# Optimization experiments

Hardware: AMD Instinct MI355X
Metric: run time of the kernel (lower is better)

The kernel has to match this reference:

```python
import jax, jax.numpy as jnp
import numpy as np

B, T, C = 2, 2048, 2048
H, HK = 16, 4          # n_head, n_kv_head (GQA)
HD = C // H            # head_dim = 128
EPS = 1e-6             # rms-norm eps


def _rope(x, cos, sin):
    # x: [B,T,h,d]; cos/sin: [T, d/2] (rotate-half RoPE)
    d2 = x.shape[-1] // 2
    x1, x2 = x[..., :d2], x[..., d2:]
    c = cos[None, :, None, :]
    s = sin[None, :, None, :]
    return jnp.concatenate([x1 * c - x2 * s, x1 * s + x2 * c], axis=-1)


def _rms(x):
    # weightless QK-norm (F.rms_norm over last dim)
    return x * jax.lax.rsqrt(jnp.mean(x * x, axis=-1, keepdims=True) + EPS)


def setup_inputs() -> dict:
    key = jax.random.key(0)
    ks = jax.random.split(key, 6)
    x = jax.random.normal(ks[0], (B, T, C), dtype=jnp.float32)
    # realistic RoPE tables
    inv_freq = 1.0 / (10000.0 ** (jnp.arange(0, HD, 2, dtype=jnp.float32) / HD))  # [HD/2]
    ang = jnp.arange(T, dtype=jnp.float32)[:, None] * inv_freq[None, :]           # [T, HD/2]
    cos, sin = jnp.cos(ang), jnp.sin(ang)
    std = 0.02
    Wq = jax.random.normal(ks[1], (C, H * HD), dtype=jnp.float32) * std
    Wk = jax.random.normal(ks[2], (C, HK * HD), dtype=jnp.float32) * std
    Wv = jax.random.normal(ks[3], (C, HK * HD), dtype=jnp.float32) * std
    Wproj = jax.random.normal(ks[4], (C, C), dtype=jnp.float32) * std
    mix1 = jnp.float32(1.0)
    mix2 = jnp.float32(0.5)
    return {"x": x, "cos": cos, "sin": sin, "Wq": Wq, "Wk": Wk, "Wv": Wv,
            "Wproj": Wproj, "mix1": mix1, "mix2": mix2}


def reference(x, cos, sin, Wq, Wk, Wv, Wproj, mix1, mix2):
    Bx, Tx, Cx = x.shape
    q = (x @ Wq).reshape(Bx, Tx, H, HD)
    k = (x @ Wk).reshape(Bx, Tx, HK, HD)
    v = (x @ Wv).reshape(Bx, Tx, HK, HD)
    q = _rms(_rope(q, cos, sin))
    k = _rms(_rope(k, cos, sin))
    q = q.transpose(0, 2, 1, 3)  # [B,H,T,D]
    k = k.transpose(0, 2, 1, 3)  # [B,HK,T,D]
    v = v.transpose(0, 2, 1, 3)
    rep = H // HK
    k = jnp.repeat(k, rep, axis=1)  # GQA repeat -> [B,H,T,D]
    v = jnp.repeat(v, rep, axis=1)
    att = jnp.einsum('bhqd,bhkd->bhqk', q, k) * (1.0 / np.sqrt(HD))
    mask = jnp.tril(jnp.ones((Tx, Tx), dtype=bool))
    att = jnp.where(mask[None, None], att, -jnp.inf)
    att = jax.nn.softmax(att, axis=-1)
    y1 = att @ v            # first-order attention output
    y2 = att @ y1           # second-order simplicial mixing (reuses att)
    y = mix1 * y1 + mix2 * y2
    y = y.transpose(0, 2, 1, 3).reshape(Bx, Tx, Cx)
    return y @ Wproj
```

## Files before the change

### kernel.cpp

```cpp
#include <hip/hip_runtime.h>
#include <hip/hip_bf16.h>
#include <cstdint>
#include <cstddef>

#define AS1 __attribute__((address_space(1)))
#define AS3 __attribute__((address_space(3)))

typedef __attribute__((ext_vector_type(8))) short bf16x8;
typedef __attribute__((ext_vector_type(4))) float f32x4;

__device__ __forceinline__ void gload_lds16(const void* g, void* l) {
  __builtin_amdgcn_global_load_lds((const AS1 void*)g, (AS3 void*)l, 16, 0, 0);
}

#define MFMA_BF16(A, B, C) __builtin_amdgcn_mfma_f32_16x16x32_bf16((A), (B), (C), 0, 0, 0)

#define QSCALE 0.12751744f
#define SMAX 16.5f

__device__ __forceinline__ uint32_t pk2(float a, float b) {
  uint32_t ua = (uint32_t)__builtin_bit_cast(unsigned short, __float2bfloat16(a));
  uint32_t ub = (uint32_t)__builtin_bit_cast(unsigned short, __float2bfloat16(b));
  return ua | (ub << 16);
}
// ... 150 lines not shown
#pragma unroll
    for (int qq = 0; qq < 16; ++qq)
      w[qq] = *(const uint2*)(CL4 + (((th * 16 + qq) * 133 + col) << 2));
    __hip_bfloat16* dstv = vb + (size_t)col * 2048 + t0 + th * 64;
#pragma unroll
    for (int e = 0; e < 8; ++e)
      *(uint4*)(dstv + e * 8) = make_uint4(w[2 * e].x, w[2 * e].y, w[2 * e + 1].x, w[2 * e + 1].y);
    return;
  }

  const int quad = tid >> 3, cp = tid & 7;
  const int tb = t0 + quad * 4;
  bf16x8 lov[4], hiv[4];
#pragma unroll
  for (int e = 0; e < 4; ++e) {
    lov[e] = *(const bf16x8*)(CL4 + ((quad * 133 + cp * 8 + e * 2) << 2));
    hiv[e] = *(const bf16x8*)(CL4 + ((quad * 133 + 64 + cp * 8 + e * 2) << 2));
  }
  const float oscale = (col0 < 2048) ? QSCALE : 1.0f;
  __hip_bfloat16* dstq = (col0 < 2048)
      ? qT + (size_t)(b * 16 + (col0 >> 7)) * 2048 * 128
      : kT + (size_t)(b * 4 + ((col0 - 2048) >> 7)) * 2048 * 128;

  float o1v[4][8], o2v[4][8], ssum[4];
#pragma unroll
  for (int rr = 0; rr < 4; ++rr) {
    const float* cb = cosb + (size_t)(tb + rr) * 64 + cp * 8;
    const float* sb = sinb + (size_t)(tb + rr) * 64 + cp * 8;
    float4 c0 = *(const float4*)cb, c1 = *(const float4*)(cb + 4);
    float4 s0 = *(const float4*)sb, s1 = *(const float4*)(sb + 4);
    float cc[8] = {c0.x, c0.y, c0.z, c0.w, c1.x, c1.y, c1.z, c1.w};
    float sn[8] = {s0.x, s0.y, s0.z, s0.w, s1.x, s1.y, s1.z, s1.w};
    float ss = 0.f;
#pragma unroll
    for (int e = 0; e < 4; ++e)
#pragma unroll
      for (int w2 = 0; w2 < 2; ++w2) {
        int pd = e * 2 + w2;
        float x1 = b2f((unsigned short)lov[e][w2 * 4 + rr]);
        float x2 = b2f((unsigned short)hiv[e][w2 * 4 + rr]);
        float a = x1 * cc[pd] - x2 * sn[pd];
        float bb = x1 * sn[pd] + x2 * cc[pd];
        o1v[rr][pd] = a;
        o2v[rr][pd] = bb;
        ss += a * a + bb * bb;
      }
    ssum[rr] = ss;
  }
#pragma unroll
  for (int rr = 0; rr < 4; ++rr) {
    float rn = rsqrtf(red8_sum(ssum[rr]) * (1.f / 128.f) + 1e-6f) * oscale;
    __hip_bfloat16* dr = dstq + (size_t)(tb + rr) * 128 + cp * 8;
    *(uint4*)dr = make_uint4(pk2(o1v[rr][0] * rn, o1v[rr][1] * rn),
                             pk2(o1v[rr][2] * rn, o1v[rr][3] * rn),
                             pk2(o1v[rr][4] * rn, o1v[rr][5] * rn),
                             pk2(o1v[rr][6] * rn, o1v[rr][7] * rn));
    *(uint4*)(dr + 64) = make_uint4(pk2(o2v[rr][0] * rn, o2v[rr][1] * rn),
                                    pk2(o2v[rr][2] * rn, o2v[rr][3] * rn),
                                    pk2(o2v[rr][4] * rn, o2v[rr][5] * rn),
                                    pk2(o2v[rr][6] * rn, o2v[rr][7] * rn));
  }
}

__global__ __launch_bounds__(256, 2) void gemm_bf16_kernel(const __hip_bfloat16* __restrict__ A,
                                                           const __hip_bfloat16* __restrict__ Bt,
                                                           float* __restrict__ C,
                                                           int M, int N, int K) {
  __shared__ __align__(16) char smem[65536];
  const int tid = threadIdx.x;
  const int lane = tid & 63;
  const int wid = tid >> 6;
  const int wm = wid >> 1, wn = wid & 1;
  const int nwg = gridDim.x;
  const int bid = blockIdx.x;
  const int swz = (bid & 7) * (nwg >> 3) + (bid >> 3);
  const int ntile = N >> 7;
  const int tm = swz / ntile, tn = swz % ntile;
  const int row0 = tm << 7, col0 = tn << 7;
  const int fr = lane & 15, hi = lane >> 4;

  auto STAGE = [&](int buf, int k0) {
#pragma unroll
    for (int i = 0; i < 4; ++i) {
      int f = i * 256 + tid;
      int r = f >> 3, s = f & 7, sx = s ^ (r & 7);
      gload_lds16(A + (size_t)(row0 + r) * K + k0 + sx * 8,
                  smem + buf * 16384 + f * 16);
    }
#pragma unroll
    for (int i = 0; i < 4; ++i) {
      int f = i * 256 + tid;
      int r = f >> 3, s = f & 7, sx = s ^ (r & 7);
      gload_lds16(Bt + (size_t)(col0 + r) * K + k0 + sx * 8,
                  smem + 32768 + buf * 16384 + f * 16);
    }
  };

  f32x4 acc[4][4] = {};
  const int nk = K >> 6;
  STAGE(0, 0);
  int cur = 0;
  for (int kk = 0; kk < nk; ++kk) {
    if (kk > 0) __builtin_amdgcn_s_barrier();
    __builtin_amdgcn_sched_barrier(0);
    if (kk + 1 < nk) STAGE(cur ^ 1, (kk + 1) * 64);
    __builtin_amdgcn_sched_barrier(0);
    if (kk + 1 < nk) asm volatile("s_waitcnt vmcnt(8)" ::: "memory");
    else             asm volatile("s_waitcnt vmcnt(0)" ::: "memory");
    __builtin_amdgcn_s_barrier();
    __builtin_amdgcn_sched_barrier(0);
    const char* Ac = smem + cur * 16384;
    const char* Bc = smem + 32768 + cur * 16384;
#pragma unroll
    for (int kh = 0; kh < 2; ++kh) {
      bf16x8 af[4], bfr[4];
#pragma unroll
      for (int n = 0; n < 4; ++n) {
        int rowb = wn * 64 + n * 16 + fr;
        int sl = (kh * 4 + hi) ^ (rowb & 7);
        bfr[n] = *(const bf16x8*)(Bc + rowb * 128 + sl * 16);
      }
#pragma unroll
      for (int m = 0; m < 4; ++m) {
        int rowa = wm * 64 + m * 16 + fr;
        int sl = (kh * 4 + hi) ^ (rowa & 7);
        af[m] = *(const bf16x8*)(Ac + rowa * 128 + sl * 16);
      }
      __builtin_amdgcn_s_setprio(1);
#pragma unroll
      for (int m = 0; m < 4; ++m)
#pragma unroll
        for (int n = 0; n < 4; ++n)
          acc[m][n] = MFMA_BF16(af[m], bfr[n], acc[m][n]);
      __builtin_amdgcn_s_setprio(0);
    }
    cur ^= 1;
  }

  const int cr = hi * 4;
#pragma unroll
  for (int m = 0; m < 4; ++m)
#pragma unroll
    for (int n = 0; n < 4; ++n) {
      int col = col0 + wn * 64 + n * 16 + fr;
#pragma unroll
      for (int r = 0; r < 4; ++r) {
        int row = row0 + wm * 64 + m * 16 + cr + r;
        C[(size_t)row * N + col] = acc[m][n][r];
      }
    }
}


__global__ __launch_bounds__(256, 2) void attn_pass1_kernel(
    const __hip_bfloat16* __restrict__ qT,
    const __hip_bfloat16* __restrict__ kT,
    const __hip_bfloat16* __restrict__ vt,
    __hip_bfloat16* __restrict__ y1u,
    float* __restrict__ Lb,
    const float* __restrict__ mix1p,
    const float* __restrict__ mix2p) {
  __shared__ __align__(16) __hip_bfloat16 Ks[2][64 * 128];
  __shared__ __align__(16) __hip_bfloat16 Vs[2][128 * 64];
  __shared__ __align__(16) char Ps[4][32 * 128];
  const int tid = threadIdx.x, lane = tid & 63, wid = tid >> 6;
  const int bi = blockIdx.x;
  const int u = bi & 255, half = bi >> 8;
  const int g = u & 7;
  const int pslot = (u >> 3) & 7;
  const int bh = g * 4 + (u >> 6);
  const int j = half ? (15 - pslot) : pslot;
  const int q0 = j * 128;
  const int nt = 2 * j + 2;
  const int sd = 2 * j + (wid >> 1);
  const __hip_bfloat16* Kp = kT + (size_t)g * 2048 * 128;
  const __hip_bfloat16* Vp = vt + (size_t)g * 128 * 2048;
  const int fr = lane & 15, hi = lane >> 4;

  bf16x8 qf[2][4];
  {
    const __hip_bfloat16* Qp = qT + ((size_t)bh * 2048 + q0 + wid * 32) * 128;
#pragma unroll
    for (int rr = 0; rr < 2; ++rr)
#pragma unroll
      for (int dc = 0; dc < 4; ++dc)
        qf[rr][dc] = *(const bf16x8*)(Qp + (rr * 16 + fr) * 128 + dc * 32 + hi * 8);
  }

  f32x4 accO[2][8] = {};
  float l[2] = {0.f, 0.f};

  char* Pb = Ps[wid];

  auto STAGE_K = [&](int buf, int kt) {
    const int k0 = kt * 64;
#pragma unroll
    for (int i = 0; i < 4; ++i) {
      int f = i * 256 + tid;
      int r = f >> 4, s = f & 15, sx = s ^ (r & 7);
      gload_lds16(Kp + (size_t)(k0 + r) * 128 + sx * 8,
                  (char*)Ks[buf] + (i * 256 + wid * 64) * 16);
    }
  };
  auto STAGE_V = [&](int buf, int kt) {
    const int k0 = kt * 64;
#pragma unroll
    for (int i = 0; i < 4; ++i) {
      int f = i * 256 + tid;
      int r = f >> 3, s = f & 7, sx = s ^ (r & 7);
      gload_lds16(Vp + (size_t)r * 2048 + k0 + sx * 8,
                  (char*)Vs[buf] + (i * 256 + wid * 64) * 16);
    }
  };

  auto QK = [&](int t, f32x4 (&sf)[2][4]) {
    const char* Kc = (const char*)Ks[t & 1];
#pragma unroll
    for (int rr = 0; rr < 2; ++rr)
#pragma unroll
      for (int c = 0; c < 4; ++c) sf[rr][c] = (f32x4){0.f, 0.f, 0.f, 0.f};
    __builtin_amdgcn_s_setprio(1);
#pragma unroll
    for (int c = 0; c < 4; ++c) {
      const int krow = c * 16 + fr;
#pragma unroll
      for (int dc = 0; dc < 4; ++dc) {
        int slot = (dc * 4 + hi) ^ (krow & 7);
        bf16x8 kf = *(const bf16x8*)(Kc + krow * 256 + slot * 16);
        sf[0][c] = MFMA_BF16(kf, qf[0][dc], sf[0][c]);
        sf[1][c] = MFMA_BF16(kf, qf[1][dc], sf[1][c]);
      }
    }
    __builtin_amdgcn_s_setprio(0);
  };

  auto STEP = [&](int s, f32x4 (&sfC)[2][4], f32x4 (&sfN)[2][4]) {
    __builtin_amdgcn_s_barrier();
    __builtin_amdgcn_sched_barrier(0);
    if (s + 2 < nt) STAGE_K(s & 1, s + 2);
    if (s + 1 < nt) STAGE_V((s + 1) & 1, s + 1);
    __builtin_amdgcn_sched_barrier(0);
    if (s + 2 < nt)      asm volatile("s_waitcnt vmcnt(8)" ::: "memory");
    else if (s + 1 < nt) asm volatile("s_waitcnt vmcnt(4)" ::: "memory");
    else                 asm volatile("s_waitcnt vmcnt(0)" ::: "memory");
    __builtin_amdgcn_s_barrier();
    __builtin_amdgcn_sched_barrier(0);

    if (s + 1 <= sd) QK(s + 1, sfN);

    if (s <= sd) {
      if (s == sd) {
#pragma unroll
        for (int rr = 0; rr < 2; ++rr) {
          const int qq = q0 + wid * 32 + rr * 16 + fr;
#pragma unroll
          for (int c = 0; c < 4; ++c) {
            const int kb = s * 64 + c * 16 + hi * 4;
#pragma unroll
            for (int r = 0; r < 4; ++r)
              if (kb + r > qq) sfC[rr][c][r] = -1e30f;
          }
        }
      }
#pragma unroll
      for (int rr = 0; rr < 2; ++rr) {
        float rs = 0.f;
#pragma unroll
        for (int c = 0; c < 4; ++c)
#pragma unroll
          for (int r = 0; r < 4; ++r) {
            float p = __builtin_amdgcn_exp2f(sfC[rr][c][r] - SMAX);
            sfC[rr][c][r] = p;
            rs += p;
          }
        l[rr] += rs;
      }
#pragma unroll
      for (int rr = 0; rr < 2; ++rr) {
        const int row = rr * 16 + fr;
        char* Prow = Pb + row * 128;
#pragma unroll
        for (int c = 0; c < 4; ++c) {
          uint32_t w0 = pk2(sfC[rr][c][0], sfC[rr][c][1]);
          uint32_t w1 = pk2(sfC[rr][c][2], sfC[rr][c][3]);
          int sl = (c * 2 + (hi >> 1)) ^ (row & 7);
          *(uint2*)(Prow + sl * 16 + (hi & 1) * 8) = make_uint2(w0, w1);
        }
      }
      bf16x8 pf[2][2];
#pragma unroll
      for (int rr = 0; rr < 2; ++rr) {
        const int row = rr * 16 + fr;
#pragma unroll
        for (int kc = 0; kc < 2; ++kc) {
          int sl = (kc * 4 + hi) ^ (row & 7);
          pf[rr][kc] = *(const bf16x8*)(Pb + row * 128 + sl * 16);
        }
      }
      const __hip_bfloat16* Vc = Vs[s & 1];
      __builtin_amdgcn_s_setprio(1);
#pragma unroll
      for (int kc = 0; kc < 2; ++kc)
#pragma unroll
        for (int f = 0; f < 8; ++f) {
          int vrow = f * 16 + fr;
          int vslot = (kc * 4 + hi) ^ (fr & 7);
          bf16x8 vf = *(const bf16x8*)(Vc + vrow * 64 + vslot * 8);
          accO[0][f] = MFMA_BF16(pf[0][kc], vf, accO[0][f]);
          accO[1][f] = MFMA_BF16(pf[1][kc], vf, accO[1][f]);
        }
      __builtin_amdgcn_s_setprio(0);
    }
  };

  f32x4 sfA[2][4], sfB[2][4];
  STAGE_K(0, 0);
  STAGE_V(0, 0);
  STAGE_K(1, 1);
  asm volatile("s_waitcnt vmcnt(8)" ::: "memory");
  __builtin_amdgcn_s_barrier();
  __builtin_amdgcn_sched_barrier(0);
  QK(0, sfA);

  for (int s2 = 0; s2 < nt; s2 += 2) {
    STEP(s2, sfA, sfB);
    STEP(s2 + 1, sfB, sfA);
  }

  float lsum[2];
#pragma unroll
  for (int rr = 0; rr < 2; ++rr) {
    float v = l[rr];
    v += __shfl_xor(v, 16);
    v += __shfl_xor(v, 32);
    lsum[rr] = v;
  }
  const float m1v = mix1p[0], m2v = mix2p[0];
  float rlq[2][4];
#pragma unroll
  for (int rr = 0; rr < 2; ++rr) {
    float inv = 1.f / lsum[rr];
#pragma unroll
    for (int r = 0; r < 4; ++r) rlq[rr][r] = __shfl(inv, hi * 4 + r);
  }
  const int t0 = q0 + wid * 32;
#pragma unroll
  for (int rr = 0; rr < 2; ++rr) {
    const int tb = t0 + rr * 16 + hi * 4;
#pragma unroll
    for (int f = 0; f < 8; ++f) {
      const int d = f * 16 + fr;
      const ushort4 v4 = *(const ushort4*)(vt + ((size_t)g * 128 + d) * 2048 + tb);
      float u0 = m1v * b2f(v4.x) + m2v * (accO[rr][f][0] * rlq[rr][0]);
      float u1 = m1v * b2f(v4.y) + m2v * (accO[rr][f][1] * rlq[rr][1]);
      float u2 = m1v * b2f(v4.z) + m2v * (accO[rr][f][2] * rlq[rr][2]);
      float u3 = m1v * b2f(v4.w) + m2v * (accO[rr][f][3] * rlq[rr][3]);
      *(uint2*)(y1u + ((size_t)bh * 128 + d) * 2048 + tb) =
          make_uint2(pk2(u0, u1), pk2(u2, u3));
    }
  }
  if (hi == 0) {
#pragma unroll
    for (int rr = 0; rr < 2; ++rr)
      Lb[(size_t)bh * 2048 + t0 + rr * 16 + fr] = lsum[rr];
  }
}

__global__ __launch_bounds__(256, 2) void attn_pass2_kernel(
    const __hip_bfloat16* __restrict__ qT,
    const __hip_bfloat16* __restrict__ kT,
    const __hip_bfloat16* __restrict__ y1u,
    const float* __restrict__ Lb,
    __hip_bfloat16* __restrict__ ymix) {
  __shared__ __align__(16) __hip_bfloat16 Ks[2][64 * 128];
  __shared__ __align__(16) __hip_bfloat16 Vs[2][128 * 64];
  __shared__ __align__(16) char Ps[4][32 * 128];
  const int tid = threadIdx.x, lane = tid & 63, wid = tid >> 6;
  const int bi = blockIdx.x;
  const int u = bi & 255, half = bi >> 8;
  const int g = u & 7;
  const int pslot = (u >> 3) & 7;
  const int bh = g * 4 + (u >> 6);
  const int h = bh & 15, b = bh >> 4;
  const int j = half ? (15 - pslot) : pslot;
  const int q0 = j * 128;
  const int nt = 2 * j + 2;
  const int sd = 2 * j + (wid >> 1);
  const __hip_bfloat16* Kp = kT + (size_t)g * 2048 * 128;
  const __hip_bfloat16* Yp = y1u + (size_t)bh * 128 * 2048;
  const int fr = lane & 15, hi = lane >> 4;

  bf16x8 qf[2][4];
  float rl[2];
  {
    const __hip_bfloat16* Qp = qT + ((size_t)bh * 2048 + q0 + wid * 32) * 128;
#pragma unroll
    for (int rr = 0; rr < 2; ++rr)
#pragma unroll
      for (int dc = 0; dc < 4; ++dc)
        qf[rr][dc] = *(const bf16x8*)(Qp + (rr * 16 + fr) * 128 + dc * 32 + hi * 8);
    const size_t qb = (size_t)bh * 2048 + q0 + wid * 32;
    rl[0] = 1.f / Lb[qb + fr];
    rl[1] = 1.f / Lb[qb + 16 + fr];
  }

  f32x4 accO[2][8] = {};
  char* Pb = Ps[wid];

  auto STAGE_K = [&](int buf, int kt) {
    const int k0 = kt * 64;
#pragma unroll
    for (int i = 0; i < 4; ++i) {
      int f = i * 256 + tid;
      int r = f >> 4, s = f & 15, sx = s ^ (r & 7);
      gload_lds16(Kp + (size_t)(k0 + r) * 128 + sx * 8,
                  (char*)Ks[buf] + (i * 256 + wid * 64) * 16);
    }
  };
  auto STAGE_V = [&](int buf, int kt) {
    const int k0 = kt * 64;
#pragma unroll
    for (int i = 0; i < 4; ++i) {
      int f = i * 256 + tid;
      int r = f >> 3, s = f & 7, sx = s ^ (r & 7);
      gload_lds16(Yp + (size_t)r * 2048 + k0 + sx * 8,
                  (char*)Vs[buf] + (i * 256 + wid * 64) * 16);
    }
  };

  auto QK = [&](int t, f32x4 (&sf)[2][4]) {
    const char* Kc = (const char*)Ks[t & 1];
#pragma unroll
    for (int rr = 0; rr < 2; ++rr)
#pragma unroll
      for (int c = 0; c < 4; ++c) sf[rr][c] = (f32x4){0.f, 0.f, 0.f, 0.f};
    __builtin_amdgcn_s_setprio(1);
#pragma unroll
    for (int c = 0; c < 4; ++c) {
      const int krow = c * 16 + fr;
#pragma unroll
      for (int dc = 0; dc < 4; ++dc) {
        int slot = (dc * 4 + hi) ^ (krow & 7);
        bf16x8 kf = *(const bf16x8*)(Kc + krow * 256 + slot * 16);
        sf[0][c] = MFMA_BF16(kf, qf[0][dc], sf[0][c]);
        sf[1][c] = MFMA_BF16(kf, qf[1][dc], sf[1][c]);
      }
    }
    __builtin_amdgcn_s_setprio(0);
  };

  auto STEP = [&](int s, f32x4 (&sfC)[2][4], f32x4 (&sfN)[2][4]) {
    __builtin_amdgcn_s_barrier();
    __builtin_amdgcn_sched_barrier(0);
    if (s + 2 < nt) STAGE_K(s & 1, s + 2);
    if (s + 1 < nt) STAGE_V((s + 1) & 1, s + 1);
    __builtin_amdgcn_sched_barrier(0);
    if (s + 2 < nt)      asm volatile("s_waitcnt vmcnt(8)" ::: "memory");
    else if (s + 1 < nt) asm volatile("s_waitcnt vmcnt(4)" ::: "memory");
    else                 asm volatile("s_waitcnt vmcnt(0)" ::: "memory");
    __builtin_amdgcn_s_barrier();
    __builtin_amdgcn_sched_barrier(0);

    if (s + 1 <= sd) QK(s + 1, sfN);

    if (s <= sd) {
      if (s == sd) {
#pragma unroll
        for (int rr = 0; rr < 2; ++rr) {
          const int qq = q0 + wid * 32 + rr * 16 + fr;
#pragma unroll
          for (int c = 0; c < 4; ++c) {
            const int kb = s * 64 + c * 16 + hi * 4;
#pragma unroll
            for (int r = 0; r < 4; ++r)
              if (kb + r > qq) sfC[rr][c][r] = -1e30f;
          }
        }
      }
#pragma unroll
      for (int rr = 0; rr < 2; ++rr)
#pragma unroll
        for (int c = 0; c < 4; ++c)
#pragma unroll
          for (int r = 0; r < 4; ++r)
            sfC[rr][c][r] = __builtin_amdgcn_exp2f(sfC[rr][c][r] - SMAX) * rl[rr];
#pragma unroll
      for (int rr = 0; rr < 2; ++rr) {
        const int row = rr * 16 + fr;
        char* Prow = Pb + row * 128;
#pragma unroll
        for (int c = 0; c < 4; ++c) {
          uint32_t w0 = pk2(sfC[rr][c][0], sfC[rr][c][1]);
          uint32_t w1 = pk2(sfC[rr][c][2], sfC[rr][c][3]);
          int sl = (c * 2 + (hi >> 1)) ^ (row & 7);
          *(uint2*)(Prow + sl * 16 + (hi & 1) * 8) = make_uint2(w0, w1);
        }
      }
      bf16x8 pf[2][2];
#pragma unroll
      for (int rr = 0; rr < 2; ++rr) {
        const int row = rr * 16 + fr;
#pragma unroll
        for (int kc = 0; kc < 2; ++kc) {
          int sl = (kc * 4 + hi) ^ (row & 7);
          pf[rr][kc] = *(const bf16x8*)(Pb + row * 128 + sl * 16);
        }
      }
      const __hip_bfloat16* Vc = Vs[s & 1];
      __builtin_amdgcn_s_setprio(1);
#pragma unroll
      for (int kc = 0; kc < 2; ++kc)
#pragma unroll
        for (int f = 0; f < 8; ++f) {
          int vrow = f * 16 + fr;
          int vslot = (kc * 4 + hi) ^ (fr & 7);
          bf16x8 vf = *(const bf16x8*)(Vc + vrow * 64 + vslot * 8);
          accO[0][f] = MFMA_BF16(pf[0][kc], vf, accO[0][f]);
          accO[1][f] = MFMA_BF16(pf[1][kc], vf, accO[1][f]);
        }
      __builtin_amdgcn_s_setprio(0);
    }
  };

  f32x4 sfA[2][4], sfB[2][4];
  STAGE_K(0, 0);
  STAGE_V(0, 0);
  STAGE_K(1, 1);
  asm volatile("s_waitcnt vmcnt(8)" ::: "memory");
  __builtin_amdgcn_s_barrier();
  __builtin_amdgcn_sched_barrier(0);
  QK(0, sfA);

  for (int s2 = 0; s2 < nt; s2 += 2) {
    STEP(s2, sfA, sfB);
    STEP(s2 + 1, sfB, sfA);
  }

#pragma unroll
  for (int rr = 0; rr < 2; ++rr) {
#pragma unroll
    for (int f = 0; f < 8; ++f) {
      const int d = f * 16 + fr;
#pragma unroll
      for (int r = 0; r < 4; ++r) {
        int q = q0 + wid * 32 + rr * 16 + hi * 4 + r;
        ymix[((size_t)b * 2048 + q) * 2048 + h * 128 + d] = __float2bfloat16(accO[rr][f][r]);
      }
    }
  }
}

extern "C" void kernel_launch(void* const* d_in, const int* in_sizes, int n_in,
                              void* d_out, int out_size, void* d_ws, size_t ws_size,
                              hipStream_t stream) {
  const float* x    = (const float*)d_in[0];
  const float* cosb = (const float*)d_in[1];
  const float* sinb = (const float*)d_in[2];
  const float* Wq   = (const float*)d_in[3];
  const float* Wk   = (const float*)d_in[4];
  const float* Wv   = (const float*)d_in[5];
  const float* Wp   = (const float*)d_in[6];
  const float* mix1 = (const float*)d_in[7];
  const float* mix2 = (const float*)d_in[8];
  float* out = (float*)d_out;
  char* ws = (char*)d_ws;

  __hip_bfloat16* xb   = (__hip_bfloat16*)(ws + 0);
  __hip_bfloat16* WTa  = (__hip_bfloat16*)(ws + 16777216);
  __hip_bfloat16* WpT  = (__hip_bfloat16*)(ws + 29360128);
  __hip_bfloat16* y1u  = (__hip_bfloat16*)(ws + 37748736);
  float*          Lb   = (float*)(ws + 54525952);
  __hip_bfloat16* qTb  = (__hip_bfloat16*)(ws + 55050240);
  __hip_bfloat16* kTb  = (__hip_bfloat16*)(ws + 71827456);
  __hip_bfloat16* vtb  = (__hip_bfloat16*)(ws + 76021760);
  __hip_bfloat16* ymix = (__hip_bfloat16*)(ws + 0);

  dim3 tb(32, 8);
  prep_kernel<<<18432, tb, 0, stream>>>(x, xb, Wq, Wk, Wv, Wp, WTa, WpT);

  gemm_qkv_rope_kernel<<<768, 256, 0, stream>>>(xb, WTa, cosb, sinb, qTb, kTb, vtb);

  attn_pass1_kernel<<<512, 256, 0, stream>>>(qTb, kTb, vtb, y1u, Lb, mix1, mix2);
  attn_pass2_kernel<<<512, 256, 0, stream>>>(qTb, kTb, y1u, Lb, ymix);

  gemm_bf16_kernel<<<512, 256, 0, stream>>>(ymix, WpT, out, 4096, 2048, 2048);
}
```

Before: 232.8 us.

## Pair causal query blocks j and 15-j in one 512-thread attention workgroup

Each attention workgroup now has 8 waves and handles two query blocks, j and 15-j. Both blocks share one stream of K/V (or y1) tiles staged in LDS, and the grid shrinks from 512 to 256 blocks. The aim is to balance causal work across workgroups and to load each shared key tile once for two query blocks. The previous software pipeline, which computed QK one step ahead, is dropped for a simpler single-stage loop, so QK latency may be exposed and there are fewer, larger blocks in flight.

```diff
diff --git a/kernel.cpp b/kernel.cpp
--- a/kernel.cpp
+++ b/kernel.cpp
@@ -326,7 +326,7 @@
 }
 
 
-__global__ __launch_bounds__(256, 2) void attn_pass1_kernel(
+__global__ __launch_bounds__(512, 2) void attn_pass1_kernel(
     const __hip_bfloat16* __restrict__ qT,
     const __hip_bfloat16* __restrict__ kT,
     const __hip_bfloat16* __restrict__ vt,
@@ -336,24 +336,24 @@
     const float* __restrict__ mix2p) {
   __shared__ __align__(16) __hip_bfloat16 Ks[2][64 * 128];
   __shared__ __align__(16) __hip_bfloat16 Vs[2][128 * 64];
-  __shared__ __align__(16) char Ps[4][32 * 128];
-  const int tid = threadIdx.x, lane = tid & 63, wid = tid >> 6;
+  __shared__ __align__(16) char Ps[8][32 * 128];
+  const int tid = threadIdx.x, lane = tid & 63, w = tid >> 6;
   const int bi = blockIdx.x;
-  const int u = bi & 255, half = bi >> 8;
-  const int g = u & 7;
-  const int pslot = (u >> 3) & 7;
-  const int bh = g * 4 + (u >> 6);
-  const int j = half ? (15 - pslot) : pslot;
-  const int q0 = j * 128;
-  const int nt = 2 * j + 2;
-  const int sd = 2 * j + (wid >> 1);
+  const int g = bi & 7;
+  const int j = (bi >> 3) & 7;
+  const int bh = g * 4 + ((bi >> 6) & 3);
+  const int ww = w & 3;
+  const int qblk = (w < 4) ? j : (15 - j);
+  const int q0 = qblk * 128;
+  const int sd = 2 * qblk + (ww >> 1);
+  const int nsteps = 32 - 2 * j;
   const __hip_bfloat16* Kp = kT + (size_t)g * 2048 * 128;
   const __hip_bfloat16* Vp = vt + (size_t)g * 128 * 2048;
   const int fr = lane & 15, hi = lane >> 4;
 
   bf16x8 qf[2][4];
   {
-    const __hip_bfloat16* Qp = qT + ((size_t)bh * 2048 + q0 + wid * 32) * 128;
+    const __hip_bfloat16* Qp = qT + ((size_t)bh * 2048 + q0 + ww * 32) * 128;
 #pragma unroll
     for (int rr = 0; rr < 2; ++rr)
 #pragma unroll
@@ -363,76 +363,63 @@
 
   f32x4 accO[2][8] = {};
   float l[2] = {0.f, 0.f};
-
-  char* Pb = Ps[wid];
-
-  auto STAGE_K = [&](int buf, int kt) {
+  char* Pb = Ps[w];
+
+  auto STAGE = [&](int buf, int kt) {
     const int k0 = kt * 64;
 #pragma unroll
-    for (int i = 0; i < 4; ++i) {
-      int f = i * 256 + tid;
+    for (int i = 0; i < 2; ++i) {
+      int f = i * 512 + tid;
       int r = f >> 4, s = f & 15, sx = s ^ (r & 7);
       gload_lds16(Kp + (size_t)(k0 + r) * 128 + sx * 8,
-                  (char*)Ks[buf] + (i * 256 + wid * 64) * 16);
-    }
-  };
-  auto STAGE_V = [&](int buf, int kt) {
-    const int k0 = kt * 64;
-#pragma unroll
-    for (int i = 0; i < 4; ++i) {
-      int f = i * 256 + tid;
+                  (char*)Ks[buf] + (i * 512 + w * 64) * 16);
+    }
+#pragma unroll
+    for (int i = 0; i < 2; ++i) {
+      int f = i * 512 + tid;
       int r = f >> 3, s = f & 7, sx = s ^ (r & 7);
       gload_lds16(Vp + (size_t)r * 2048 + k0 + sx * 8,
-                  (char*)Vs[buf] + (i * 256 + wid * 64) * 16);
+                  (char*)Vs[buf] + (i * 512 + w * 64) * 16);
     }
   };
 
-  auto QK = [&](int t, f32x4 (&sf)[2][4]) {
-    const char* Kc = (const char*)Ks[t & 1];
-#pragma unroll
-    for (int rr = 0; rr < 2; ++rr)
-#pragma unroll
-      for (int c = 0; c < 4; ++c) sf[rr][c] = (f32x4){0.f, 0.f, 0.f, 0.f};
-    __builtin_amdgcn_s_setprio(1);
-#pragma unroll
-    for (int c = 0; c < 4; ++c) {
-      const int krow = c * 16 + fr;
-#pragma unroll
-      for (int dc = 0; dc < 4; ++dc) {
-        int slot = (dc * 4 + hi) ^ (krow & 7);
-        bf16x8 kf = *(const bf16x8*)(Kc + krow * 256 + slot * 16);
-        sf[0][c] = MFMA_BF16(kf, qf[0][dc], sf[0][c]);
-        sf[1][c] = MFMA_BF16(kf, qf[1][dc], sf[1][c]);
-      }
-    }
-    __builtin_amdgcn_s_setprio(0);
-  };
-
-  auto STEP = [&](int s, f32x4 (&sfC)[2][4], f32x4 (&sfN)[2][4]) {
+  STAGE(0, 0);
+  for (int s = 0; s < nsteps; ++s) {
+    if (s > 0) __builtin_amdgcn_s_barrier();
+    __builtin_amdgcn_sched_barrier(0);
+    if (s + 1 < nsteps) STAGE((s + 1) & 1, s + 1);
+    __builtin_amdgcn_sched_barrier(0);
+    if (s + 1 < nsteps) asm volatile("s_waitcnt vmcnt(4)" ::: "memory");
+    else                asm volatile("s_waitcnt vmcnt(0)" ::: "memory");
     __builtin_amdgcn_s_barrier();
     __builtin_amdgcn_sched_barrier(0);
-    if (s + 2 < nt) STAGE_K(s & 1, s + 2);
-    if (s + 1 < nt) STAGE_V((s + 1) & 1, s + 1);
-    __builtin_amdgcn_sched_barrier(0);
-    if (s + 2 < nt)      asm volatile("s_waitcnt vmcnt(8)" ::: "memory");
-    else if (s + 1 < nt) asm volatile("s_waitcnt vmcnt(4)" ::: "memory");
-    else                 asm volatile("s_waitcnt vmcnt(0)" ::: "memory");
-    __builtin_amdgcn_s_barrier();
-    __builtin_amdgcn_sched_barrier(0);
-
-    if (s + 1 <= sd) QK(s + 1, sfN);
 
     if (s <= sd) {
+      const char* Kc = (const char*)Ks[s & 1];
+      f32x4 sf[2][4] = {};
+      __builtin_amdgcn_s_setprio(1);
+#pragma unroll
+      for (int c = 0; c < 4; ++c) {
+        const int krow = c * 16 + fr;
+#pragma unroll
+        for (int dc = 0; dc < 4; ++dc) {
+          int slot = (dc * 4 + hi) ^ (krow & 7);
+          bf16x8 kf = *(const bf16x8*)(Kc + krow * 256 + slot * 16);
+          sf[0][c] = MFMA_BF16(kf, qf[0][dc], sf[0][c]);
+          sf[1][c] = MFMA_BF16(kf, qf[1][dc], sf[1][c]);
+        }
+      }
+      __builtin_amdgcn_s_setprio(0);
       if (s == sd) {
 #pragma unroll
         for (int rr = 0; rr < 2; ++rr) {
-          const int qq = q0 + wid * 32 + rr * 16 + fr;
+          const int qq = q0 + ww * 32 + rr * 16 + fr;
 #pragma unroll
           for (int c = 0; c < 4; ++c) {
             const int kb = s * 64 + c * 16 + hi * 4;
 #pragma unroll
             for (int r = 0; r < 4; ++r)
-              if (kb + r > qq) sfC[rr][c][r] = -1e30f;
+              if (kb + r > qq) sf[rr][c][r] = -1e30f;
           }
         }
       }
@@ -443,8 +430,8 @@
         for (int c = 0; c < 4; ++c)
 #pragma unroll
           for (int r = 0; r < 4; ++r) {
-            float p = __builtin_amdgcn_exp2f(sfC[rr][c][r] - SMAX);
-            sfC[rr][c][r] = p;
+            float p = __builtin_amdgcn_exp2f(sf[rr][c][r] - SMAX);
+            sf[rr][c][r] = p;
             rs += p;
           }
         l[rr] += rs;
@@ -455,8 +442,8 @@
         char* Prow = Pb + row * 128;
 #pragma unroll
         for (int c = 0; c < 4; ++c) {
-          uint32_t w0 = pk2(sfC[rr][c][0], sfC[rr][c][1]);
-          uint32_t w1 = pk2(sfC[rr][c][2], sfC[rr][c][3]);
+          uint32_t w0 = pk2(sf[rr][c][0], sf[rr][c][1]);
+          uint32_t w1 = pk2(sf[rr][c][2], sf[rr][c][3]);
           int sl = (c * 2 + (hi >> 1)) ^ (row & 7);
           *(uint2*)(Prow + sl * 16 + (hi & 1) * 8) = make_uint2(w0, w1);
         }
@@ -485,20 +472,6 @@
         }
       __builtin_amdgcn_s_setprio(0);
     }
-  };
-
-  f32x4 sfA[2][4], sfB[2][4];
-  STAGE_K(0, 0);
-  STAGE_V(0, 0);
-  STAGE_K(1, 1);
-  asm volatile("s_waitcnt vmcnt(8)" ::: "memory");
-  __builtin_amdgcn_s_barrier();
-  __builtin_amdgcn_sched_barrier(0);
-  QK(0, sfA);
-
-  for (int s2 = 0; s2 < nt; s2 += 2) {
-    STEP(s2, sfA, sfB);
-    STEP(s2 + 1, sfB, sfA);
   }
 
   float lsum[2];
@@ -517,7 +490,7 @@
 #pragma unroll
     for (int r = 0; r < 4; ++r) rlq[rr][r] = __shfl(inv, hi * 4 + r);
   }
-  const int t0 = q0 + wid * 32;
+  const int t0 = q0 + ww * 32;
 #pragma unroll
   for (int rr = 0; rr < 2; ++rr) {
     const int tb = t0 + rr * 16 + hi * 4;
@@ -540,7 +513,7 @@
   }
 }
 
-__global__ __launch_bounds__(256, 2) void attn_pass2_kernel(
+__global__ __launch_bounds__(512, 2) void attn_pass2_kernel(
     const __hip_bfloat16* __restrict__ qT,
     const __hip_bfloat16* __restrict__ kT,
     const __hip_bfloat16* __restrict__ y1u,
@@ -548,18 +521,18 @@
     __hip_bfloat16* __restrict__ ymix) {
   __shared__ __align__(16) __hip_bfloat16 Ks[2][64 * 128];
   __shared__ __align__(16) __hip_bfloat16 Vs[2][128 * 64];
-  __shared__ __align__(16) char Ps[4][32 * 128];
-  const int tid = threadIdx.x, lane = tid & 63, wid = tid >> 6;
+  __shared__ __align__(16) char Ps[8][32 * 128];
+  const int tid = threadIdx.x, lane = tid & 63, w = tid >> 6;
   const int bi = blockIdx.x;
-  const int u = bi & 255, half = bi >> 8;
-  const int g = u & 7;
-  const int pslot = (u >> 3) & 7;
-  const int bh = g * 4 + (u >> 6);
+  const int g = bi & 7;
+  const int j = (bi >> 3) & 7;
+  const int bh = g * 4 + ((bi >> 6) & 3);
   const int h = bh & 15, b = bh >> 4;
-  const int j = half ? (15 - pslot) : pslot;
-  const int q0 = j * 128;
-  const int nt = 2 * j + 2;
-  const int sd = 2 * j + (wid >> 1);
+  const int ww = w & 3;
+  const int qblk = (w < 4) ? j : (15 - j);
+  const int q0 = qblk * 128;
+  const int sd = 2 * qblk + (ww >> 1);
+  const int nsteps = 32 - 2 * j;
   const __hip_bfloat16* Kp = kT + (size_t)g * 2048 * 128;
   const __hip_bfloat16* Yp = y1u + (size_t)bh * 128 * 2048;
   const int fr = lane & 15, hi = lane >> 4;
@@ -567,87 +540,75 @@
   bf16x8 qf[2][4];
   float rl[2];
   {
-    const __hip_bfloat16* Qp = qT + ((size_t)bh * 2048 + q0 + wid * 32) * 128;
+    const __hip_bfloat16* Qp = qT + ((size_t)bh * 2048 + q0 + ww * 32) * 128;
 #pragma unroll
     for (int rr = 0; rr < 2; ++rr)
 #pragma unroll
       for (int dc = 0; dc < 4; ++dc)
         qf[rr][dc] = *(const bf16x8*)(Qp + (rr * 16 + fr) * 128 + dc * 32 + hi * 8);
-    const size_t qb = (size_t)bh * 2048 + q0 + wid * 32;
+    const size_t qb = (size_t)bh * 2048 + q0 + ww * 32;
     rl[0] = 1.f / Lb[qb + fr];
     rl[1] = 1.f / Lb[qb + 16 + fr];
   }
 
   f32x4 accO[2][8] = {};
-  char* Pb = Ps[wid];
-
-  auto STAGE_K = [&](int buf, int kt) {
+  char* Pb = Ps[w];
+
+  auto STAGE = [&](int buf, int kt) {
     const int k0 = kt * 64;
 #pragma unroll
-    for (int i = 0; i < 4; ++i) {
-      int f = i * 256 + tid;
+    for (int i = 0; i < 2; ++i) {
+      int f = i * 512 + tid;
       int r = f >> 4, s = f & 15, sx = s ^ (r & 7);
       gload_lds16(Kp + (size_t)(k0 + r) * 128 + sx * 8,
-                  (char*)Ks[buf] + (i * 256 + wid * 64) * 16);
-    }
-  };
-  auto STAGE_V = [&](int buf, int kt) {
-    const int k0 = kt * 64;
-#pragma unroll
-    for (int i = 0; i < 4; ++i) {
-      int f = i * 256 + tid;
+                  (char*)Ks[buf] + (i * 512 + w * 64) * 16);
+    }
+#pragma unroll
+    for (int i = 0; i < 2; ++i) {
+      int f = i * 512 + tid;
       int r = f >> 3, s = f & 7, sx = s ^ (r & 7);
       gload_lds16(Yp + (size_t)r * 2048 + k0 + sx * 8,
-                  (char*)Vs[buf] + (i * 256 + wid * 64) * 16);
+                  (char*)Vs[buf] + (i * 512 + w * 64) * 16);
     }
   };
 
-  auto QK = [&](int t, f32x4 (&sf)[2][4]) {
-    const char* Kc = (const char*)Ks[t & 1];
-#pragma unroll
-    for (int rr = 0; rr < 2; ++rr)
-#pragma unroll
-      for (int c = 0; c < 4; ++c) sf[rr][c] = (f32x4){0.f, 0.f, 0.f, 0.f};
-    __builtin_amdgcn_s_setprio(1);
-#pragma unroll
-    for (int c = 0; c < 4; ++c) {
-      const int krow = c * 16 + fr;
-#pragma unroll
-      for (int dc = 0; dc < 4; ++dc) {
-        int slot = (dc * 4 + hi) ^ (krow & 7);
-        bf16x8 kf = *(const bf16x8*)(Kc + krow * 256 + slot * 16);
-        sf[0][c] = MFMA_BF16(kf, qf[0][dc], sf[0][c]);
-        sf[1][c] = MFMA_BF16(kf, qf[1][dc], sf[1][c]);
-      }
-    }
-    __builtin_amdgcn_s_setprio(0);
-  };
-
-  auto STEP = [&](int s, f32x4 (&sfC)[2][4], f32x4 (&sfN)[2][4]) {
+  STAGE(0, 0);
+  for (int s = 0; s < nsteps; ++s) {
+    if (s > 0) __builtin_amdgcn_s_barrier();
+    __builtin_amdgcn_sched_barrier(0);
+    if (s + 1 < nsteps) STAGE((s + 1) & 1, s + 1);
+    __builtin_amdgcn_sched_barrier(0);
+    if (s + 1 < nsteps) asm volatile("s_waitcnt vmcnt(4)" ::: "memory");
+    else                asm volatile("s_waitcnt vmcnt(0)" ::: "memory");
     __builtin_amdgcn_s_barrier();
     __builtin_amdgcn_sched_barrier(0);
-    if (s + 2 < nt) STAGE_K(s & 1, s + 2);
-    if (s + 1 < nt) STAGE_V((s + 1) & 1, s + 1);
-    __builtin_amdgcn_sched_barrier(0);
-    if (s + 2 < nt)      asm volatile("s_waitcnt vmcnt(8)" ::: "memory");
-    else if (s + 1 < nt) asm volatile("s_waitcnt vmcnt(4)" ::: "memory");
-    else                 asm volatile("s_waitcnt vmcnt(0)" ::: "memory");
-    __builtin_amdgcn_s_barrier();
-    __builtin_amdgcn_sched_barrier(0);
-
-    if (s + 1 <= sd) QK(s + 1, sfN);
 
     if (s <= sd) {
+      const char* Kc = (const char*)Ks[s & 1];
+      f32x4 sf[2][4] = {};
+      __builtin_amdgcn_s_setprio(1);
+#pragma unroll
+      for (int c = 0; c < 4; ++c) {
+        const int krow = c * 16 + fr;
+#pragma unroll
+        for (int dc = 0; dc < 4; ++dc) {
+          int slot = (dc * 4 + hi) ^ (krow & 7);
+          bf16x8 kf = *(const bf16x8*)(Kc + krow * 256 + slot * 16);
+          sf[0][c] = MFMA_BF16(kf, qf[0][dc], sf[0][c]);
+          sf[1][c] = MFMA_BF16(kf, qf[1][dc], sf[1][c]);
+        }
+      }
+      __builtin_amdgcn_s_setprio(0);
       if (s == sd) {
 #pragma unroll
         for (int rr = 0; rr < 2; ++rr) {
-          const int qq = q0 + wid * 32 + rr * 16 + fr;
+          const int qq = q0 + ww * 32 + rr * 16 + fr;
 #pragma unroll
           for (int c = 0; c < 4; ++c) {
             const int kb = s * 64 + c * 16 + hi * 4;
 #pragma unroll
             for (int r = 0; r < 4; ++r)
-              if (kb + r > qq) sfC[rr][c][r] = -1e30f;
+              if (kb + r > qq) sf[rr][c][r] = -1e30f;
           }
         }
       }
@@ -657,15 +618,15 @@
         for (int c = 0; c < 4; ++c)
 #pragma unroll
           for (int r = 0; r < 4; ++r)
-            sfC[rr][c][r] = __builtin_amdgcn_exp2f(sfC[rr][c][r] - SMAX) * rl[rr];
+            sf[rr][c][r] = __builtin_amdgcn_exp2f(sf[rr][c][r] - SMAX) * rl[rr];
 #pragma unroll
       for (int rr = 0; rr < 2; ++rr) {
         const int row = rr * 16 + fr;
         char* Prow = Pb + row * 128;
 #pragma unroll
         for (int c = 0; c < 4; ++c) {
-          uint32_t w0 = pk2(sfC[rr][c][0], sfC[rr][c][1]);
-          uint32_t w1 = pk2(sfC[rr][c][2], sfC[rr][c][3]);
+          uint32_t w0 = pk2(sf[rr][c][0], sf[rr][c][1]);
+          uint32_t w1 = pk2(sf[rr][c][2], sf[rr][c][3]);
           int sl = (c * 2 + (hi >> 1)) ^ (row & 7);
           *(uint2*)(Prow + sl * 16 + (hi & 1) * 8) = make_uint2(w0, w1);
         }
@@ -694,20 +655,6 @@
         }
       __builtin_amdgcn_s_setprio(0);
     }
-  };
-
-  f32x4 sfA[2][4], sfB[2][4];
-  STAGE_K(0, 0);
-  STAGE_V(0, 0);
-  STAGE_K(1, 1);
-  asm volatile("s_waitcnt vmcnt(8)" ::: "memory");
-  __builtin_amdgcn_s_barrier();
-  __builtin_amdgcn_sched_barrier(0);
-  QK(0, sfA);
-
-  for (int s2 = 0; s2 < nt; s2 += 2) {
-    STEP(s2, sfA, sfB);
-    STEP(s2 + 1, sfB, sfA);
   }
 
 #pragma unroll
@@ -717,7 +664,7 @@
       const int d = f * 16 + fr;
 #pragma unroll
       for (int r = 0; r < 4; ++r) {
-        int q = q0 + wid * 32 + rr * 16 + hi * 4 + r;
+        int q = q0 + ww * 32 + rr * 16 + hi * 4 + r;
         ymix[((size_t)b * 2048 + q) * 2048 + h * 128 + d] = __float2bfloat16(accO[rr][f][r]);
       }
     }
@@ -754,8 +701,8 @@
 
   gemm_qkv_rope_kernel<<<768, 256, 0, stream>>>(xb, WTa, cosb, sinb, qTb, kTb, vtb);
 
-  attn_pass1_kernel<<<512, 256, 0, stream>>>(qTb, kTb, vtb, y1u, Lb, mix1, mix2);
-  attn_pass2_kernel<<<512, 256, 0, stream>>>(qTb, kTb, y1u, Lb, ymix);
+  attn_pass1_kernel<<<256, 512, 0, stream>>>(qTb, kTb, vtb, y1u, Lb, mix1, mix2);
+  attn_pass2_kernel<<<256, 512, 0, stream>>>(qTb, kTb, y1u, Lb, ymix);
 
   gemm_bf16_kernel<<<512, 256, 0, stream>>>(ymix, WpT, out, 4096, 2048, 2048);
 }
```

Result: slower. 239.3 us (+2.8%).

## Replace software-pipelined QK prefetch with simple single-stage K/V double buffering

Applied to the files above, without the earlier changes.

Both attention kernels drop the pipeline that computed QK for tile s+1 while doing PV for tile s, with K staged two tiles ahead. K and V are now staged together one tile ahead, and QK, softmax and PV for each tile run in sequence inside a plain loop. This frees the second score register set, which can lower register pressure and raise occupancy. The cost is less overlap between the QK MFMAs and the softmax/PV work, and less lead time for the K loads.

```diff
diff --git a/kernel.cpp b/kernel.cpp
--- a/kernel.cpp
+++ b/kernel.cpp
@@ -366,7 +366,7 @@
 
   char* Pb = Ps[wid];
 
-  auto STAGE_K = [&](int buf, int kt) {
+  auto STAGE = [&](int buf, int kt) {
     const int k0 = kt * 64;
 #pragma unroll
     for (int i = 0; i < 4; ++i) {
@@ -375,9 +375,6 @@
       gload_lds16(Kp + (size_t)(k0 + r) * 128 + sx * 8,
                   (char*)Ks[buf] + (i * 256 + wid * 64) * 16);
     }
-  };
-  auto STAGE_V = [&](int buf, int kt) {
-    const int k0 = kt * 64;
 #pragma unroll
     for (int i = 0; i < 4; ++i) {
       int f = i * 256 + tid;
@@ -387,42 +384,33 @@
     }
   };
 
-  auto QK = [&](int t, f32x4 (&sf)[2][4]) {
-    const char* Kc = (const char*)Ks[t & 1];
-#pragma unroll
-    for (int rr = 0; rr < 2; ++rr)
-#pragma unroll
-      for (int c = 0; c < 4; ++c) sf[rr][c] = (f32x4){0.f, 0.f, 0.f, 0.f};
-    __builtin_amdgcn_s_setprio(1);
-#pragma unroll
-    for (int c = 0; c < 4; ++c) {
-      const int krow = c * 16 + fr;
-#pragma unroll
-      for (int dc = 0; dc < 4; ++dc) {
-        int slot = (dc * 4 + hi) ^ (krow & 7);
-        bf16x8 kf = *(const bf16x8*)(Kc + krow * 256 + slot * 16);
-        sf[0][c] = MFMA_BF16(kf, qf[0][dc], sf[0][c]);
-        sf[1][c] = MFMA_BF16(kf, qf[1][dc], sf[1][c]);
-      }
-    }
-    __builtin_amdgcn_s_setprio(0);
-  };
-
-  auto STEP = [&](int s, f32x4 (&sfC)[2][4], f32x4 (&sfN)[2][4]) {
+  STAGE(0, 0);
+  for (int s = 0; s < nt; ++s) {
+    if (s > 0) __builtin_amdgcn_s_barrier();
+    __builtin_amdgcn_sched_barrier(0);
+    if (s + 1 < nt) STAGE((s + 1) & 1, s + 1);
+    __builtin_amdgcn_sched_barrier(0);
+    if (s + 1 < nt) asm volatile("s_waitcnt vmcnt(8)" ::: "memory");
+    else            asm volatile("s_waitcnt vmcnt(0)" ::: "memory");
     __builtin_amdgcn_s_barrier();
     __builtin_amdgcn_sched_barrier(0);
-    if (s + 2 < nt) STAGE_K(s & 1, s + 2);
-    if (s + 1 < nt) STAGE_V((s + 1) & 1, s + 1);
-    __builtin_amdgcn_sched_barrier(0);
-    if (s + 2 < nt)      asm volatile("s_waitcnt vmcnt(8)" ::: "memory");
-    else if (s + 1 < nt) asm volatile("s_waitcnt vmcnt(4)" ::: "memory");
-    else                 asm volatile("s_waitcnt vmcnt(0)" ::: "memory");
-    __builtin_amdgcn_s_barrier();
-    __builtin_amdgcn_sched_barrier(0);
-
-    if (s + 1 <= sd) QK(s + 1, sfN);
 
     if (s <= sd) {
+      const char* Kc = (const char*)Ks[s & 1];
+      f32x4 sf[2][4] = {};
+      __builtin_amdgcn_s_setprio(1);
+#pragma unroll
+      for (int c = 0; c < 4; ++c) {
+        const int krow = c * 16 + fr;
+#pragma unroll
+        for (int dc = 0; dc < 4; ++dc) {
+          int slot = (dc * 4 + hi) ^ (krow & 7);
+          bf16x8 kf = *(const bf16x8*)(Kc + krow * 256 + slot * 16);
+          sf[0][c] = MFMA_BF16(kf, qf[0][dc], sf[0][c]);
+          sf[1][c] = MFMA_BF16(kf, qf[1][dc], sf[1][c]);
+        }
+      }
+      __builtin_amdgcn_s_setprio(0);
       if (s == sd) {
 #pragma unroll
         for (int rr = 0; rr < 2; ++rr) {
@@ -432,7 +420,7 @@
             const int kb = s * 64 + c * 16 + hi * 4;
 #pragma unroll
             for (int r = 0; r < 4; ++r)
-              if (kb + r > qq) sfC[rr][c][r] = -1e30f;
+              if (kb + r > qq) sf[rr][c][r] = -1e30f;
           }
         }
       }
@@ -443,8 +431,8 @@
         for (int c = 0; c < 4; ++c)
 #pragma unroll
           for (int r = 0; r < 4; ++r) {
-            float p = __builtin_amdgcn_exp2f(sfC[rr][c][r] - SMAX);
-            sfC[rr][c][r] = p;
+            float p = __builtin_amdgcn_exp2f(sf[rr][c][r] - SMAX);
+            sf[rr][c][r] = p;
             rs += p;
           }
         l[rr] += rs;
@@ -455,8 +443,8 @@
         char* Prow = Pb + row * 128;
 #pragma unroll
         for (int c = 0; c < 4; ++c) {
-          uint32_t w0 = pk2(sfC[rr][c][0], sfC[rr][c][1]);
-          uint32_t w1 = pk2(sfC[rr][c][2], sfC[rr][c][3]);
+          uint32_t w0 = pk2(sf[rr][c][0], sf[rr][c][1]);
+          uint32_t w1 = pk2(sf[rr][c][2], sf[rr][c][3]);
           int sl = (c * 2 + (hi >> 1)) ^ (row & 7);
           *(uint2*)(Prow + sl * 16 + (hi & 1) * 8) = make_uint2(w0, w1);
         }
@@ -485,20 +473,6 @@
         }
       __builtin_amdgcn_s_setprio(0);
     }
-  };
-
-  f32x4 sfA[2][4], sfB[2][4];
-  STAGE_K(0, 0);
-  STAGE_V(0, 0);
-  STAGE_K(1, 1);
-  asm volatile("s_waitcnt vmcnt(8)" ::: "memory");
-  __builtin_amdgcn_s_barrier();
-  __builtin_amdgcn_sched_barrier(0);
-  QK(0, sfA);
-
-  for (int s2 = 0; s2 < nt; s2 += 2) {
-    STEP(s2, sfA, sfB);
-    STEP(s2 + 1, sfB, sfA);
   }
 
   float lsum[2];
@@ -581,7 +555,7 @@
   f32x4 accO[2][8] = {};
   char* Pb = Ps[wid];
 
-  auto STAGE_K = [&](int buf, int kt) {
+  auto STAGE = [&](int buf, int kt) {
     const int k0 = kt * 64;
 #pragma unroll
     for (int i = 0; i < 4; ++i) {
@@ -590,9 +564,6 @@
       gload_lds16(Kp + (size_t)(k0 + r) * 128 + sx * 8,
                   (char*)Ks[buf] + (i * 256 + wid * 64) * 16);
     }
-  };
-  auto STAGE_V = [&](int buf, int kt) {
-    const int k0 = kt * 64;
 #pragma unroll
     for (int i = 0; i < 4; ++i) {
       int f = i * 256 + tid;
@@ -602,42 +573,33 @@
     }
   };
 
-  auto QK = [&](int t, f32x4 (&sf)[2][4]) {
-    const char* Kc = (const char*)Ks[t & 1];
-#pragma unroll
-    for (int rr = 0; rr < 2; ++rr)
-#pragma unroll
-      for (int c = 0; c < 4; ++c) sf[rr][c] = (f32x4){0.f, 0.f, 0.f, 0.f};
-    __builtin_amdgcn_s_setprio(1);
-#pragma unroll
-    for (int c = 0; c < 4; ++c) {
-      const int krow = c * 16 + fr;
-#pragma unroll
-      for (int dc = 0; dc < 4; ++dc) {
-        int slot = (dc * 4 + hi) ^ (krow & 7);
-        bf16x8 kf = *(const bf16x8*)(Kc + krow * 256 + slot * 16);
-        sf[0][c] = MFMA_BF16(kf, qf[0][dc], sf[0][c]);
-        sf[1][c] = MFMA_BF16(kf, qf[1][dc], sf[1][c]);
-      }
-    }
-    __builtin_amdgcn_s_setprio(0);
-  };
-
-  auto STEP = [&](int s, f32x4 (&sfC)[2][4], f32x4 (&sfN)[2][4]) {
+  STAGE(0, 0);
+  for (int s = 0; s < nt; ++s) {
+    if (s > 0) __builtin_amdgcn_s_barrier();
+    __builtin_amdgcn_sched_barrier(0);
+    if (s + 1 < nt) STAGE((s + 1) & 1, s + 1);
+    __builtin_amdgcn_sched_barrier(0);
+    if (s + 1 < nt) asm volatile("s_waitcnt vmcnt(8)" ::: "memory");
+    else            asm volatile("s_waitcnt vmcnt(0)" ::: "memory");
     __builtin_amdgcn_s_barrier();
     __builtin_amdgcn_sched_barrier(0);
-    if (s + 2 < nt) STAGE_K(s & 1, s + 2);
-    if (s + 1 < nt) STAGE_V((s + 1) & 1, s + 1);
-    __builtin_amdgcn_sched_barrier(0);
-    if (s + 2 < nt)      asm volatile("s_waitcnt vmcnt(8)" ::: "memory");
-    else if (s + 1 < nt) asm volatile("s_waitcnt vmcnt(4)" ::: "memory");
-    else                 asm volatile("s_waitcnt vmcnt(0)" ::: "memory");
-    __builtin_amdgcn_s_barrier();
-    __builtin_amdgcn_sched_barrier(0);
-
-    if (s + 1 <= sd) QK(s + 1, sfN);
 
     if (s <= sd) {
+      const char* Kc = (const char*)Ks[s & 1];
+      f32x4 sf[2][4] = {};
+      __builtin_amdgcn_s_setprio(1);
+#pragma unroll
+      for (int c = 0; c < 4; ++c) {
+        const int krow = c * 16 + fr;
+#pragma unroll
+        for (int dc = 0; dc < 4; ++dc) {
+          int slot = (dc * 4 + hi) ^ (krow & 7);
+          bf16x8 kf = *(const bf16x8*)(Kc + krow * 256 + slot * 16);
+          sf[0][c] = MFMA_BF16(kf, qf[0][dc], sf[0][c]);
+          sf[1][c] = MFMA_BF16(kf, qf[1][dc], sf[1][c]);
+        }
+      }
+      __builtin_amdgcn_s_setprio(0);
       if (s == sd) {
 #pragma unroll
         for (int rr = 0; rr < 2; ++rr) {
@@ -647,7 +609,7 @@
             const int kb = s * 64 + c * 16 + hi * 4;
 #pragma unroll
             for (int r = 0; r < 4; ++r)
-              if (kb + r > qq) sfC[rr][c][r] = -1e30f;
+              if (kb + r > qq) sf[rr][c][r] = -1e30f;
           }
         }
       }
@@ -657,15 +619,15 @@
         for (int c = 0; c < 4; ++c)
 #pragma unroll
           for (int r = 0; r < 4; ++r)
-            sfC[rr][c][r] = __builtin_amdgcn_exp2f(sfC[rr][c][r] - SMAX) * rl[rr];
+            sf[rr][c][r] = __builtin_amdgcn_exp2f(sf[rr][c][r] - SMAX) * rl[rr];
 #pragma unroll
       for (int rr = 0; rr < 2; ++rr) {
         const int row = rr * 16 + fr;
         char* Prow = Pb + row * 128;
 #pragma unroll
         for (int c = 0; c < 4; ++c) {
-          uint32_t w0 = pk2(sfC[rr][c][0], sfC[rr][c][1]);
-          uint32_t w1 = pk2(sfC[rr][c][2], sfC[rr][c][3]);
+          uint32_t w0 = pk2(sf[rr][c][0], sf[rr][c][1]);
+          uint32_t w1 = pk2(sf[rr][c][2], sf[rr][c][3]);
           int sl = (c * 2 + (hi >> 1)) ^ (row & 7);
           *(uint2*)(Prow + sl * 16 + (hi & 1) * 8) = make_uint2(w0, w1);
         }
@@ -694,20 +656,6 @@
         }
       __builtin_amdgcn_s_setprio(0);
     }
-  };
-
-  f32x4 sfA[2][4], sfB[2][4];
-  STAGE_K(0, 0);
-  STAGE_V(0, 0);
-  STAGE_K(1, 1);
-  asm volatile("s_waitcnt vmcnt(8)" ::: "memory");
-  __builtin_amdgcn_s_barrier();
-  __builtin_amdgcn_sched_barrier(0);
-  QK(0, sfA);
-
-  for (int s2 = 0; s2 < nt; s2 += 2) {
-    STEP(s2, sfA, sfB);
-    STEP(s2 + 1, sfB, sfA);
   }
 
 #pragma unroll
```

Measured after the change: 233.8 us. About the same (+0.4%).

## Simplify first attention pass pipeline and defer softmax normalization in second pass

Applied to the files above, without the earlier changes.

The first attention kernel drops its software-pipelined schedule, where QK for the next tile overlapped the current PV and K was prefetched two tiles ahead. It now uses a simple single-step double-buffered loop that stages K and V together and runs QK then PV within each tile. Separately, the second-pass kernel stops multiplying each probability by the row reciprocal before the bf16 pack and instead scales the accumulator once at output. This saves per-element multiplies in the second pass and lowers register pressure in the first, at the cost of less MFMA/softmax overlap and slightly different bf16 rounding of unnormalized probabilities.

```diff
diff --git a/kernel.cpp b/kernel.cpp
--- a/kernel.cpp
+++ b/kernel.cpp
@@ -366,7 +366,7 @@
 
   char* Pb = Ps[wid];
 
-  auto STAGE_K = [&](int buf, int kt) {
+  auto STAGE = [&](int buf, int kt) {
     const int k0 = kt * 64;
 #pragma unroll
     for (int i = 0; i < 4; ++i) {
@@ -375,9 +375,6 @@
       gload_lds16(Kp + (size_t)(k0 + r) * 128 + sx * 8,
                   (char*)Ks[buf] + (i * 256 + wid * 64) * 16);
     }
-  };
-  auto STAGE_V = [&](int buf, int kt) {
-    const int k0 = kt * 64;
 #pragma unroll
     for (int i = 0; i < 4; ++i) {
       int f = i * 256 + tid;
@@ -387,42 +384,33 @@
     }
   };
 
-  auto QK = [&](int t, f32x4 (&sf)[2][4]) {
-    const char* Kc = (const char*)Ks[t & 1];
-#pragma unroll
-    for (int rr = 0; rr < 2; ++rr)
-#pragma unroll
-      for (int c = 0; c < 4; ++c) sf[rr][c] = (f32x4){0.f, 0.f, 0.f, 0.f};
-    __builtin_amdgcn_s_setprio(1);
-#pragma unroll
-    for (int c = 0; c < 4; ++c) {
-      const int krow = c * 16 + fr;
-#pragma unroll
-      for (int dc = 0; dc < 4; ++dc) {
-        int slot = (dc * 4 + hi) ^ (krow & 7);
-        bf16x8 kf = *(const bf16x8*)(Kc + krow * 256 + slot * 16);
-        sf[0][c] = MFMA_BF16(kf, qf[0][dc], sf[0][c]);
-        sf[1][c] = MFMA_BF16(kf, qf[1][dc], sf[1][c]);
-      }
-    }
-    __builtin_amdgcn_s_setprio(0);
-  };
-
-  auto STEP = [&](int s, f32x4 (&sfC)[2][4], f32x4 (&sfN)[2][4]) {
+  STAGE(0, 0);
+  for (int s = 0; s < nt; ++s) {
+    if (s > 0) __builtin_amdgcn_s_barrier();
+    __builtin_amdgcn_sched_barrier(0);
+    if (s + 1 < nt) STAGE((s + 1) & 1, s + 1);
+    __builtin_amdgcn_sched_barrier(0);
+    if (s + 1 < nt) asm volatile("s_waitcnt vmcnt(8)" ::: "memory");
+    else            asm volatile("s_waitcnt vmcnt(0)" ::: "memory");
     __builtin_amdgcn_s_barrier();
     __builtin_amdgcn_sched_barrier(0);
-    if (s + 2 < nt) STAGE_K(s & 1, s + 2);
-    if (s + 1 < nt) STAGE_V((s + 1) & 1, s + 1);
-    __builtin_amdgcn_sched_barrier(0);
-    if (s + 2 < nt)      asm volatile("s_waitcnt vmcnt(8)" ::: "memory");
-    else if (s + 1 < nt) asm volatile("s_waitcnt vmcnt(4)" ::: "memory");
-    else                 asm volatile("s_waitcnt vmcnt(0)" ::: "memory");
-    __builtin_amdgcn_s_barrier();
-    __builtin_amdgcn_sched_barrier(0);
-
-    if (s + 1 <= sd) QK(s + 1, sfN);
 
     if (s <= sd) {
+      const char* Kc = (const char*)Ks[s & 1];
+      f32x4 sf[2][4] = {};
+      __builtin_amdgcn_s_setprio(1);
+#pragma unroll
+      for (int c = 0; c < 4; ++c) {
+        const int krow = c * 16 + fr;
+#pragma unroll
+        for (int dc = 0; dc < 4; ++dc) {
+          int slot = (dc * 4 + hi) ^ (krow & 7);
+          bf16x8 kf = *(const bf16x8*)(Kc + krow * 256 + slot * 16);
+          sf[0][c] = MFMA_BF16(kf, qf[0][dc], sf[0][c]);
+          sf[1][c] = MFMA_BF16(kf, qf[1][dc], sf[1][c]);
+        }
+      }
+      __builtin_amdgcn_s_setprio(0);
       if (s == sd) {
 #pragma unroll
         for (int rr = 0; rr < 2; ++rr) {
@@ -432,7 +420,7 @@
             const int kb = s * 64 + c * 16 + hi * 4;
 #pragma unroll
             for (int r = 0; r < 4; ++r)
-              if (kb + r > qq) sfC[rr][c][r] = -1e30f;
+              if (kb + r > qq) sf[rr][c][r] = -1e30f;
           }
         }
       }
@@ -443,8 +431,8 @@
         for (int c = 0; c < 4; ++c)
 #pragma unroll
           for (int r = 0; r < 4; ++r) {
-            float p = __builtin_amdgcn_exp2f(sfC[rr][c][r] - SMAX);
-            sfC[rr][c][r] = p;
+            float p = __builtin_amdgcn_exp2f(sf[rr][c][r] - SMAX);
+            sf[rr][c][r] = p;
             rs += p;
           }
         l[rr] += rs;
@@ -455,8 +443,8 @@
         char* Prow = Pb + row * 128;
 #pragma unroll
         for (int c = 0; c < 4; ++c) {
-          uint32_t w0 = pk2(sfC[rr][c][0], sfC[rr][c][1]);
-          uint32_t w1 = pk2(sfC[rr][c][2], sfC[rr][c][3]);
+          uint32_t w0 = pk2(sf[rr][c][0], sf[rr][c][1]);
+          uint32_t w1 = pk2(sf[rr][c][2], sf[rr][c][3]);
           int sl = (c * 2 + (hi >> 1)) ^ (row & 7);
           *(uint2*)(Prow + sl * 16 + (hi & 1) * 8) = make_uint2(w0, w1);
         }
@@ -485,20 +473,6 @@
         }
       __builtin_amdgcn_s_setprio(0);
     }
-  };
-
-  f32x4 sfA[2][4], sfB[2][4];
-  STAGE_K(0, 0);
-  STAGE_V(0, 0);
-  STAGE_K(1, 1);
-  asm volatile("s_waitcnt vmcnt(8)" ::: "memory");
-  __builtin_amdgcn_s_barrier();
-  __builtin_amdgcn_sched_barrier(0);
-  QK(0, sfA);
-
-  for (int s2 = 0; s2 < nt; s2 += 2) {
-    STEP(s2, sfA, sfB);
-    STEP(s2 + 1, sfB, sfA);
   }
 
   float lsum[2];
@@ -657,7 +631,7 @@
         for (int c = 0; c < 4; ++c)
 #pragma unroll
           for (int r = 0; r < 4; ++r)
-            sfC[rr][c][r] = __builtin_amdgcn_exp2f(sfC[rr][c][r] - SMAX) * rl[rr];
+            sfC[rr][c][r] = __builtin_amdgcn_exp2f(sfC[rr][c][r] - SMAX);
 #pragma unroll
       for (int rr = 0; rr < 2; ++rr) {
         const int row = rr * 16 + fr;
@@ -710,6 +684,11 @@
     STEP(s2 + 1, sfB, sfA);
   }
 
+  float rlq[2][4];
+#pragma unroll
+  for (int rr = 0; rr < 2; ++rr)
+#pragma unroll
+    for (int r = 0; r < 4; ++r) rlq[rr][r] = __shfl(rl[rr], hi * 4 + r);
 #pragma unroll
   for (int rr = 0; rr < 2; ++rr) {
 #pragma unroll
@@ -718,7 +697,8 @@
 #pragma unroll
       for (int r = 0; r < 4; ++r) {
         int q = q0 + wid * 32 + rr * 16 + hi * 4 + r;
-        ymix[((size_t)b * 2048 + q) * 2048 + h * 128 + d] = __float2bfloat16(accO[rr][f][r]);
+        ymix[((size_t)b * 2048 + q) * 2048 + h * 128 + d] =
+            __float2bfloat16(accO[rr][f][r] * rlq[rr][r]);
       }
     }
   }
```

Result: no change. 231.1 us, median of 2 (-0.7%).
